# Optimization experiments

Measured on AMD Instinct MI355X. Metric: run time of the kernel, lower is better.

Reference implementation:

```python
import jax, jax.numpy as jnp
import numpy as np

L, B, N, DIM, H, DH, MLP = 2, 4, 2048, 768, 12, 64, 3072


def layer_norm(x, g, eps=1e-5):
    m = jnp.mean(x, axis=-1, keepdims=True)
    v = jnp.mean((x - m) ** 2, axis=-1, keepdims=True)
    return (x - m) / jnp.sqrt(v + eps) * g


def rms_norm(x, g):
    # F.normalize(x, dim=-1) * sqrt(dim_head) * gamma ; gamma: [H,1,DH]
    n = jnp.linalg.norm(x, axis=-1, keepdims=True)
    return x / jnp.maximum(n, 1e-12) * (x.shape[-1] ** 0.5) * g


def rotate_half(x):
    x1, x2 = jnp.split(x, 2, axis=-1)
    return jnp.concatenate([-x2, x1], axis=-1)


def apply_2d_rope(q, k, h_idx, w_idx):
    D = q.shape[-1]
    dq = D // 4
    inv_freq = 1.0 / (10000.0 ** (jnp.arange(dq, dtype=jnp.float32) / dq))

    def sincos(idx):
        th = idx[..., None].astype(jnp.float32) * inv_freq  # [B,N,dq]
        s = jnp.concatenate([jnp.sin(th), jnp.sin(th)], axis=-1)[:, None, :, :]
        c = jnp.concatenate([jnp.cos(th), jnp.cos(th)], axis=-1)[:, None, :, :]
        return s, c

    sh, ch = sincos(h_idx)
    sw, cw = sincos(w_idx)

    def rope(x, s, c):
        return x * c + rotate_half(x) * s

    dh = D // 2
    q = jnp.concatenate([rope(q[..., :dh], sh, ch), rope(q[..., dh:], sw, cw)], axis=-1)
    k = jnp.concatenate([rope(k[..., :dh], sh, ch), rope(k[..., dh:], sw, cw)], axis=-1)
    return q, k


def setup_inputs() -> dict:
    key = jax.random.key(0)
    ks = jax.random.split(key, 20)
    s = 0.02
    inp = {
        "patches": jax.random.normal(ks[0], (B, N, DIM), jnp.float32),
        "pe_ln1_g": jnp.ones((DIM,), jnp.float32),
        "pe_W": jax.random.normal(ks[1], (DIM, DIM), jnp.float32) * s,
        "pe_b": jnp.zeros((DIM,), jnp.float32),
        "pe_ln2_g": jnp.ones((DIM,), jnp.float32),
        "attn_ln_g": jnp.ones((L, DIM), jnp.float32),
        "qn_g": jnp.ones((L, H, 1, DH), jnp.float32),
        "kn_g": jnp.ones((L, H, 1, DH), jnp.float32),
        "Wq": jax.random.normal(ks[2], (L, DIM, H * DH), jnp.float32) * s,
        "Wkv": jax.random.normal(ks[3], (L, DIM, 2 * H * DH), jnp.float32) * s,
        "Wo": jax.random.normal(ks[4], (L, H * DH, DIM), jnp.float32) * s,
        "ff_ln_g": jnp.ones((L, DIM), jnp.float32),
        "W1": jax.random.normal(ks[5], (L, DIM, MLP), jnp.float32) * s,
        "b1": jnp.zeros((L, MLP), jnp.float32),
        "W2": jax.random.normal(ks[6], (L, MLP, DIM), jnp.float32) * s,
        "b2": jnp.zeros((L, DIM), jnp.float32),
        "final_ln_g": jnp.ones((DIM,), jnp.float32),
        "h_idx": jax.random.randint(ks[7], (B, N), 0, 64, jnp.int32),
        "w_idx": jax.random.randint(ks[8], (B, N), 0, 64, jnp.int32),
        "lengths": jax.random.randint(ks[9], (B,), 1, N + 1, jnp.int32),
    }
    return inp


def reference(patches, pe_ln1_g, pe_W, pe_b, pe_ln2_g, attn_ln_g, qn_g, kn_g,
              Wq, Wkv, Wo, ff_ln_g, W1, b1, W2, b2, final_ln_g,
              h_idx, w_idx, lengths):
    mask = jnp.arange(N)[None, :] < lengths[:, None]  # [B,N] validity mask
    # patch embedding: LN -> Linear -> LN
    x = layer_norm(patches, pe_ln1_g)
    x = x @ pe_W + pe_b
    x = layer_norm(x, pe_ln2_g)
    for i in range(L):
        xn = layer_norm(x, attn_ln_g[i])
        q = (xn @ Wq[i]).reshape(B, N, H, DH).transpose(0, 2, 1, 3)
        kv = xn @ Wkv[i]
        k = kv[..., : H * DH].reshape(B, N, H, DH).transpose(0, 2, 1, 3)
        v = kv[..., H * DH:].reshape(B, N, H, DH).transpose(0, 2, 1, 3)
        q = rms_norm(q, qn_g[i])
        k = rms_norm(k, kn_g[i])
        q, k = apply_2d_rope(q, k, h_idx, w_idx)
        dots = jnp.einsum('bhid,bhjd->bhij', q, k)  # no 1/sqrt(d): QK-RMSNorm supplies scale
        neg = -jnp.finfo(dots.dtype).max
        dots = jnp.where(mask[:, None, None, :], dots, neg)
        attn = jax.nn.softmax(dots, axis=-1)
        out = jnp.einsum('bhij,bhjd->bhid', attn, v)
        out = out.transpose(0, 2, 1, 3).reshape(B, N, H * DH)
        x = out @ Wo[i] + x
        h = layer_norm(x, ff_ln_g[i])
        h = jax.nn.gelu(h @ W1[i] + b1[i], approximate=False)
        x = h @ W2[i] + b2[i] + x
    x = layer_norm(x, final_ln_g)
    return x, mask
```

## Files before the change

kernel.cpp:

```cpp
#include <hip/hip_runtime.h>
#include <math.h>

#define LNUM 2
#define BB   4
#define NN   2048
#define DIM  768
#define NH   12
#define DH   64
#define MLPD 3072
#define QKVD 2304

typedef __attribute__((ext_vector_type(8))) short bf16x8;
typedef __attribute__((ext_vector_type(4))) float f32x4;
typedef unsigned short ushort_t;

__device__ __forceinline__ ushort_t f2bf(float f) {
    union { float f; unsigned u; } v; v.f = f;
    unsigned r = v.u + 0x7fff + ((v.u >> 16) & 1);
    return (ushort_t)(r >> 16);
}
__device__ __forceinline__ float bf2f(ushort_t s) {
    union { unsigned u; float f; } v; v.u = ((unsigned)s) << 16;
    return v.f;
}
__device__ __forceinline__ void gld16(const void* g, void* l) {
    __builtin_amdgcn_global_load_lds(
        (const __attribute__((address_space(1))) void*)g,
        (__attribute__((address_space(3))) void*)l, 16, 0, 0);
}
__device__ __forceinline__ float gelu_f(float x) {
    const float y = 0.7978845608028654f * (x + 0.044715f * x * x * x);
    const float t = 1.f - 2.f / (1.f + __expf(2.f * y));
    return 0.5f * x * (1.f + t);
}

#define WOFF_L 7077888
__global__ __launch_bounds__(256) void wconvert_all_kernel(
    const float* __restrict__ peW, const float* __restrict__ Wq,
    const float* __restrict__ Wkv, const float* __restrict__ Wo,
    const float* __restrict__ W1, const float* __restrict__ W2,
    ushort_t* __restrict__ wbf)
{
    int bid = blockIdx.x;
    const float* src; ushort_t* dst; int K, N;
    if (bid < 576)        { src = peW;                      dst = wbf;                               K = 768;  N = 768;  }
    else {
        bid -= 576;
        const int layer = bid / 6912;
        int t = bid % 6912;
        const size_t lw = (size_t)layer * WOFF_L;
        if (t < 576)        {           src = Wq  + (size_t)layer * 768 * 768;   dst = wbf + 589824 + lw;           K = 768;  N = 768;  }
        else if (t < 1728)  { t -= 576; src = Wkv + (size_t)layer * 768 * 1536;  dst = wbf + 589824 + 589824 + lw;  K = 768;  N = 1536; }
        else if (t < 2304)  { t -= 1728; src = Wo + (size_t)layer * 768 * 768;   dst = wbf + 589824 + 1769472 + lw; K = 768;  N = 768;  }
        else if (t < 4608)  { t -= 2304; src = W1 + (size_t)layer * 768 * 3072;  dst = wbf + 589824 + 2359296 + lw; K = 768;  N = 3072; }
        else                { t -= 4608; src = W2 + (size_t)layer * 3072 * 768;  dst = wbf + 589824 + 4718592 + lw; K = 3072; N = 768;  }
        bid = t;
    }
    const int tilesN = N / 32;
    const int nt = (bid % tilesN) * 32, kt = (bid / tilesN) * 32;

    __shared__ ushort_t tl[32][33];
    const int tx = threadIdx.x & 31, ty = threadIdx.x >> 5;
#pragma unroll
    for (int r = 0; r < 4; r++) {
        const int k = kt + ty + r * 8;
        tl[ty + r * 8][tx] = f2bf(src[(size_t)k * N + nt + tx]);
    }
    __syncthreads();
#pragma unroll
    for (int r = 0; r < 4; r++) {
        const int n = nt + ty + r * 8;
        dst[(size_t)n * K + kt + tx] = tl[tx][ty + r * 8];
    }
}

template <typename OT>
__global__ __launch_bounds__(256) void ln_kernel(const float* in, const float* g, OT* out)
{
    const int row = blockIdx.x;
    const int tid = threadIdx.x;
    const float* rp = in + (size_t)row * DIM;
    float vals[3];
    float s = 0.f, s2 = 0.f;
#pragma unroll
    for (int k = 0; k < 3; k++) {
        float v = rp[tid + k * 256];
        vals[k] = v;
        s += v; s2 += v * v;
    }
#pragma unroll
    for (int o = 32; o; o >>= 1) {
        s  += __shfl_xor(s, o);
        s2 += __shfl_xor(s2, o);
    }
    __shared__ float red[8];
    const int wid = tid >> 6;
    if ((tid & 63) == 0) { red[wid] = s; red[wid + 4] = s2; }
    __syncthreads();
    s  = red[0] + red[1] + red[2] + red[3];
    s2 = red[4] + red[5] + red[6] + red[7];
    const float mean = s * (1.f / DIM);
    const float var  = s2 * (1.f / DIM) - mean * mean;
    const float inv  = rsqrtf(var + 1e-5f);
    OT* op = out + (size_t)row * DIM;
#pragma unroll
    for (int k = 0; k < 3; k++) {
        const float v = (vals[k] - mean) * inv * g[tid + k * 256];
        if constexpr (sizeof(OT) == 2) op[tid + k * 256] = f2bf(v);
        else                           op[tid + k * 256] = v;
    }
}

template <int TM>
__global__ __launch_bounds__(256) void gemm_bf(
    const ushort_t* __restrict__ A, const ushort_t* __restrict__ Bt,
    const float* __restrict__ bias, const float* __restrict__ resid,
    void* __restrict__ Cv, int M, int N, int K, int outbf, int act)
{
    constexpr int MF = TM / 32;
    constexpr int AG = TM / 32;
    __shared__ ushort_t As[2][TM * 64];
    __shared__ ushort_t Bs[2][128 * 64];
    const int tid  = threadIdx.x;
    const int w    = tid >> 6, lane = tid & 63;
    const int lq   = lane & 15, quad = lane >> 4;
    const int wm   = w & 1, wn = w >> 1;
    const int tileM = blockIdx.y * TM, tileN = blockIdx.x * 128;

    const int srow   = lane >> 3;
    const int schunk = (lane & 7) ^ srow;
    const ushort_t* agp[AG];
    const ushort_t* bgp[4];
#pragma unroll
    for (int g = 0; g < AG; g++)
        agp[g] = A + (size_t)(tileM + g * 32 + w * 8 + srow) * K + schunk * 8;
#pragma unroll
    for (int g = 0; g < 4; g++)
        bgp[g] = Bt + (size_t)(tileN + g * 32 + w * 8 + srow) * K + schunk * 8;

    f32x4 acc[MF][4];
#pragma unroll
    for (int m = 0; m < MF; m++)
#pragma unroll
        for (int n = 0; n < 4; n++) acc[m][n] = (f32x4){0.f, 0.f, 0.f, 0.f};

    const int fsw0 = (quad ^ (lq & 7)) * 8;
    const int fsw1 = ((quad ^ (lq & 7)) ^ 4) * 8;

#pragma unroll
    for (int g = 0; g < AG; g++)
        gld16(agp[g], As[0] + (g * 32 + w * 8) * 64);
#pragma unroll
    for (int g = 0; g < 4; g++)
        gld16(bgp[g], Bs[0] + (g * 32 + w * 8) * 64);

    int buf = 0;
    for (int kt = 0; kt < K; kt += 64, buf ^= 1) {
        if (kt + 64 < K) {
#pragma unroll
            for (int g = 0; g < AG; g++)
                gld16(agp[g] + kt + 64, As[buf ^ 1] + (g * 32 + w * 8) * 64);
#pragma unroll
            for (int g = 0; g < 4; g++)
                gld16(bgp[g] + kt + 64, Bs[buf ^ 1] + (g * 32 + w * 8) * 64);
            if constexpr (TM == 128) asm volatile("s_waitcnt vmcnt(8)" ::: "memory");
            else                     asm volatile("s_waitcnt vmcnt(6)" ::: "memory");
        } else {
            asm volatile("s_waitcnt vmcnt(0)" ::: "memory");
        }
        __builtin_amdgcn_s_barrier();

        bf16x8 af0[MF], af1[MF], bf0[4], bf1[4];
#pragma unroll
        for (int m = 0; m < MF; m++) {
            const int base = ((wm * MF + m) * 16 + lq) * 64;
            af0[m] = *(const bf16x8*)&As[buf][base + fsw0];
            af1[m] = *(const bf16x8*)&As[buf][base + fsw1];
        }
#pragma unroll
        for (int n = 0; n < 4; n++) {
            const int base = ((wn * 4 + n) * 16 + lq) * 64;
            bf0[n] = *(const bf16x8*)&Bs[buf][base + fsw0];
            bf1[n] = *(const bf16x8*)&Bs[buf][base + fsw1];
        }
#pragma unroll
        for (int n = 0; n < 4; n++)
#pragma unroll
            for (int m = 0; m < MF; m++) {
                acc[m][n] = __builtin_amdgcn_mfma_f32_16x16x32_bf16(af0[m], bf0[n], acc[m][n], 0, 0, 0);
                acc[m][n] = __builtin_amdgcn_mfma_f32_16x16x32_bf16(af1[m], bf1[n], acc[m][n], 0, 0, 0);
            }
        __builtin_amdgcn_s_barrier();
    }

    float* Cf = (float*)Cv;
    ushort_t* Cb = (ushort_t*)Cv;
#pragma unroll
    for (int m = 0; m < MF; m++) {
#pragma unroll
        for (int n = 0; n < 4; n++) {
            const int col = tileN + wn * 64 + n * 16 + lq;
            const float bv = bias ? bias[col] : 0.f;
#pragma unroll
            for (int r = 0; r < 4; r++) {
                const int row = tileM + wm * (TM / 2) + m * 16 + quad * 4 + r;
                float v = acc[m][n][r] + bv;
                if (act) v = gelu_f(v);
                const size_t off = (size_t)row * N + col;
                if (resid) v += resid[off];
                if (outbf) Cb[off] = f2bf(v);
                else       Cf[off] = v;
            }
        }
    }
}

#define ASB(b) (Sh + (b) * 8192)
#define BSB(b) (Sh + 16384 + (b) * 8192)
__global__ __launch_bounds__(256) void gemm_qkv_kernel(
    const ushort_t* __restrict__ A, const ushort_t* __restrict__ Bt,
    ushort_t* __restrict__ C, ushort_t* __restrict__ Vt,
    const float* __restrict__ qg, const float* __restrict__ kg,
    const int* __restrict__ h_idx, const int* __restrict__ w_idx,
    int M, int N, int K)
{
    constexpr int MF = 4;
    constexpr int AG = 4;
    __shared__ ushort_t Sh[32768];
    const int tid  = threadIdx.x;
    const int w    = tid >> 6, lane = tid & 63;
    const int lq   = lane & 15, quad = lane >> 4;
    const int wm   = w & 1, wn = w >> 1;
    const int tileM = blockIdx.y * 128, tileN = blockIdx.x * 128;

    const int srow   = lane >> 3;
    const int schunk = (lane & 7) ^ srow;
    const ushort_t* agp[AG];
    const ushort_t* bgp[4];
#pragma unroll
    for (int g = 0; g < AG; g++)
        agp[g] = A + (size_t)(tileM + g * 32 + w * 8 + srow) * K + schunk * 8;
#pragma unroll
    for (int g = 0; g < 4; g++)
        bgp[g] = Bt + (size_t)(tileN + g * 32 + w * 8 + srow) * K + schunk * 8;

    f32x4 acc[MF][4];
#pragma unroll
    for (int m = 0; m < MF; m++)
#pragma unroll
        for (int n = 0; n < 4; n++) acc[m][n] = (f32x4){0.f, 0.f, 0.f, 0.f};

    const int fsw0 = (quad ^ (lq & 7)) * 8;
    const int fsw1 = ((quad ^ (lq & 7)) ^ 4) * 8;

#pragma unroll
    for (int g = 0; g < AG; g++)
        gld16(agp[g], ASB(0) + (g * 32 + w * 8) * 64);
#pragma unroll
    for (int g = 0; g < 4; g++)
        gld16(bgp[g], BSB(0) + (g * 32 + w * 8) * 64);

    int buf = 0;
    for (int kt = 0; kt < K; kt += 64, buf ^= 1) {
        if (kt + 64 < K) {
#pragma unroll
            for (int g = 0; g < AG; g++)
                gld16(agp[g] + kt + 64, ASB(buf ^ 1) + (g * 32 + w * 8) * 64);
#pragma unroll
            for (int g = 0; g < 4; g++)
                gld16(bgp[g] + kt + 64, BSB(buf ^ 1) + (g * 32 + w * 8) * 64);
            asm volatile("s_waitcnt vmcnt(8)" ::: "memory");
        } else {
            asm volatile("s_waitcnt vmcnt(0)" ::: "memory");
        }
        __builtin_amdgcn_s_barrier();

        bf16x8 af0[MF], af1[MF], bf0[4], bf1[4];
#pragma unroll
        for (int m = 0; m < MF; m++) {
            const int base = ((wm * MF + m) * 16 + lq) * 64;
            af0[m] = *(const bf16x8*)&ASB(buf)[base + fsw0];
            af1[m] = *(const bf16x8*)&ASB(buf)[base + fsw1];
        }
#pragma unroll
        for (int n = 0; n < 4; n++) {
            const int base = ((wn * 4 + n) * 16 + lq) * 64;
            bf0[n] = *(const bf16x8*)&BSB(buf)[base + fsw0];
            bf1[n] = *(const bf16x8*)&BSB(buf)[base + fsw1];
        }
#pragma unroll
        for (int n = 0; n < 4; n++)
#pragma unroll
            for (int m = 0; m < MF; m++) {
                acc[m][n] = __builtin_amdgcn_mfma_f32_16x16x32_bf16(af0[m], bf0[n], acc[m][n], 0, 0, 0);
                acc[m][n] = __builtin_amdgcn_mfma_f32_16x16x32_bf16(af1[m], bf1[n], acc[m][n], 0, 0, 0);
            }
        __builtin_amdgcn_s_barrier();
    }

    const int colb = tileN + wn * 64;
    if (colb >= 2 * DIM) {
        const int h0  = (tileN - 2 * DIM) >> 6;
        const int b   = tileM >> 11;
        const int nb0 = tileM & (NN - 1);
#pragma unroll
        for (int m = 0; m < MF; m++) {
            const int ns_loc = wm * 64 + m * 16 + quad * 4;
#pragma unroll
            for (int n = 0; n < 4; n++) {
                const int rowl = wn * 64 + n * 16 + lq;
                const unsigned lo = (unsigned)f2bf(acc[m][n][0]) | ((unsigned)f2bf(acc[m][n][1]) << 16);
                const unsigned hi = (unsigned)f2bf(acc[m][n][2]) | ((unsigned)f2bf(acc[m][n][3]) << 16);
                *(uint2*)&Sh[rowl * 136 + ns_loc] = make_uint2(lo, hi);
            }
        }
        __syncthreads();
        const int chunk = tid & 15;
        const int rgrp  = tid >> 4;
#pragma unroll
        for (int pr = 0; pr < 8; pr++) {
            const int rowl = pr * 16 + rgrp;
            const int hh = rowl >> 6, d = rowl & 63;
            const uint4 v4 = *(const uint4*)&Sh[rowl * 136 + chunk * 8];
            *(uint4*)&Vt[((size_t)(b * NH + h0 + hh) * DH + d) * NN + nb0 + chunk * 8] = v4;
        }
        return;
    }

    const float* gq = (colb < DIM) ? (qg + colb) : (kg + (colb - DIM));
    float gv4[4];
#pragma unroll
    for (int n = 0; n < 4; n++) gv4[n] = gq[n * 16 + lq];
    const float freq = exp2f((float)lq * -0.8304820237218407f);

#pragma unroll
    for (int m = 0; m < MF; m++) {
#pragma unroll
        for (int r = 0; r < 4; r++) {
            const int row = tileM + wm * 64 + m * 16 + quad * 4 + r;
            float v0 = acc[m][0][r], v1 = acc[m][1][r];
            float v2 = acc[m][2][r], v3 = acc[m][3][r];
            float ss = (v0 * v0 + v1 * v1) + (v2 * v2 + v3 * v3);
            ss += __shfl_xor(ss, 1);
            ss += __shfl_xor(ss, 2);
            ss += __shfl_xor(ss, 4);
            ss += __shfl_xor(ss, 8);
            const float sc = 8.0f / fmaxf(sqrtf(ss), 1e-12f);
            v0 *= sc * gv4[0]; v1 *= sc * gv4[1];
            v2 *= sc * gv4[2]; v3 *= sc * gv4[3];
            const float th1 = (float)h_idx[row] * freq;
            const float th2 = (float)w_idx[row] * freq;
            const float s1 = __sinf(th1), c1 = __cosf(th1);
            const float s2 = __sinf(th2), c2 = __cosf(th2);
            const float o0 = v0 * c1 - v1 * s1;
            const float o1 = v1 * c1 + v0 * s1;
            const float o2 = v2 * c2 - v3 * s2;
            const float o3 = v3 * c2 + v2 * s2;
            const size_t off = (size_t)row * N + colb + lq;
            C[off]      = f2bf(o0);
            C[off + 16] = f2bf(o1);
            C[off + 32] = f2bf(o2);
            C[off + 48] = f2bf(o3);
        }
    }
}

__global__ __launch_bounds__(256) void attn_kernel(
    const ushort_t* __restrict__ QKV, const ushort_t* __restrict__ Vt_g,
    const int* __restrict__ lengths, ushort_t* __restrict__ O)
{
    __shared__ ushort_t Ks[64 * 64];
    __shared__ ushort_t Vs[64 * 64];
    __shared__ ushort_t Ps[4][16][76];

    const int bh = blockIdx.x;
    const int b  = bh / NH;
    const int h  = bh % NH;
    const int qbase = blockIdx.y * 64;
    const int tid  = threadIdx.x;
    const int w    = tid >> 6;
    const int lane = tid & 63;
    const int lq   = lane & 15;
    const int quad = lane >> 4;
    const int len  = lengths[b];

    const int qrow = qbase + w * 16 + lq;
    const ushort_t* qp = QKV + (size_t)(b * NN + qrow) * QKVD + h * DH + quad * 8;
    bf16x8 aq0 = *(const bf16x8*)(qp);
    bf16x8 aq1 = *(const bf16x8*)(qp + 32);

    const int e0 = tid, e1 = tid + 256;
    const int r0 = e0 >> 3, c80 = e0 & 7;
    const int r1 = e1 >> 3, c81 = e1 & 7;
    const int g0 = (c80 ^ (r0 & 7) ^ (r0 >> 3)) & 7;
    const int g1 = (c81 ^ (r1 & 7) ^ (r1 >> 3)) & 7;
    const ushort_t* kg0 = QKV + (size_t)(b * NN + r0) * QKVD + DIM + h * DH + g0 * 8;
    const ushort_t* kg1 = QKV + (size_t)(b * NN + r1) * QKVD + DIM + h * DH + g1 * 8;
    const ushort_t* vg0 = Vt_g + ((size_t)(b * NH + h) * DH + r0) * NN + g0 * 8;
    const ushort_t* vg1 = Vt_g + ((size_t)(b * NH + h) * DH + r1) * NN + g1 * 8;
    ushort_t* kl0 = Ks + (w * 64) * 8;
    ushort_t* kl1 = Ks + (256 + w * 64) * 8;
    ushort_t* vl0 = Vs + (w * 64) * 8;
    ushort_t* vl1 = Vs + (256 + w * 64) * 8;

    f32x4 oacc[4];
#pragma unroll
    for (int t4 = 0; t4 < 4; t4++) oacc[t4] = (f32x4){0.f, 0.f, 0.f, 0.f};
    float lsum = 0.f;

    const int ntiles = (len + 63) >> 6;
    for (int t = 0; t < ntiles; t++) {
        const int j0 = t * 64;
        gld16(kg0 + (size_t)j0 * QKVD, kl0);
        gld16(kg1 + (size_t)j0 * QKVD, kl1);
        gld16(vg0 + j0, vl0);
        gld16(vg1 + j0, vl1);
        __syncthreads();

        f32x4 s[4];
#pragma unroll
        for (int n = 0; n < 4; n++) {
            const int krow = n * 16 + lq;
            const int hashk = (krow & 7) ^ (krow >> 3);
            bf16x8 ak0 = *(const bf16x8*)&Ks[(krow * 8 + ((quad ^ hashk) & 7)) * 8];
            bf16x8 ak1 = *(const bf16x8*)&Ks[(krow * 8 + (((quad + 4) ^ hashk) & 7)) * 8];
            f32x4 acc = (f32x4){0.f, 0.f, 0.f, 0.f};
            acc = __builtin_amdgcn_mfma_f32_16x16x32_bf16(ak0, aq0, acc, 0, 0, 0);
            acc = __builtin_amdgcn_mfma_f32_16x16x32_bf16(ak1, aq1, acc, 0, 0, 0);
            s[n] = acc;
        }

        float p[4][4];
#pragma unroll
        for (int n = 0; n < 4; n++) {
            const int keyb = j0 + n * 16 + quad * 4;
#pragma unroll
            for (int r = 0; r < 4; r++) {
                float pv = __expf(s[n][r]);
                pv = (keyb + r < len) ? pv : 0.f;
                p[n][r] = pv;
                lsum += pv;
            }
        }

#pragma unroll
        for (int n = 0; n < 4; n++) {
            const unsigned lo = (unsigned)f2bf(p[n][0]) | ((unsigned)f2bf(p[n][1]) << 16);
            const unsigned hi = (unsigned)f2bf(p[n][2]) | ((unsigned)f2bf(p[n][3]) << 16);
            *(uint2*)&Ps[w][lq][n * 16 + quad * 4] = make_uint2(lo, hi);
        }
        asm volatile("s_waitcnt lgkmcnt(0)" ::: "memory");
        bf16x8 ap0 = *(const bf16x8*)&Ps[w][lq][quad * 8];
        bf16x8 ap1 = *(const bf16x8*)&Ps[w][lq][32 + quad * 8];

#pragma unroll
        for (int t4 = 0; t4 < 4; t4++) {
            const int vrow = t4 * 16 + lq;
            const int hashv = (vrow & 7) ^ (vrow >> 3);
            bf16x8 bv0 = *(const bf16x8*)&Vs[(vrow * 8 + ((quad ^ hashv) & 7)) * 8];
            bf16x8 bv1 = *(const bf16x8*)&Vs[(vrow * 8 + (((quad + 4) ^ hashv) & 7)) * 8];
            oacc[t4] = __builtin_amdgcn_mfma_f32_16x16x32_bf16(ap0, bv0, oacc[t4], 0, 0, 0);
            oacc[t4] = __builtin_amdgcn_mfma_f32_16x16x32_bf16(ap1, bv1, oacc[t4], 0, 0, 0);
        }
        __syncthreads();
    }

    lsum += __shfl_xor(lsum, 16);
    lsum += __shfl_xor(lsum, 32);
    float invq[4];
#pragma unroll
    for (int r = 0; r < 4; r++) invq[r] = 1.f / __shfl(lsum, quad * 4 + r);

#pragma unroll
    for (int t4 = 0; t4 < 4; t4++) {
#pragma unroll
        for (int r = 0; r < 4; r++) {
            const int qr = qbase + w * 16 + quad * 4 + r;
            O[((size_t)(b * NN + qr)) * DIM + h * DH + t4 * 16 + lq] = f2bf(oacc[t4][r] * invq[r]);
        }
    }
}

__global__ __launch_bounds__(256) void mask_kernel(const int* __restrict__ lengths, float* __restrict__ out)
{
    const int i = blockIdx.x * 256 + threadIdx.x;
    const int b = i >> 11;
    const int n = i & (NN - 1);
    out[i] = (n < lengths[b]) ? 1.f : 0.f;
}

extern "C" void kernel_launch(void* const* d_in, const int* in_sizes, int n_in,
                              void* d_out, int out_size, void* d_ws, size_t ws_size,
                              hipStream_t stream)
{
    const float* patches    = (const float*)d_in[0];
    const float* pe_ln1_g   = (const float*)d_in[1];
    const float* pe_W       = (const float*)d_in[2];
    const float* pe_b       = (const float*)d_in[3];
    const float* pe_ln2_g   = (const float*)d_in[4];
    const float* attn_ln_g  = (const float*)d_in[5];
    const float* qn_g       = (const float*)d_in[6];
    const float* kn_g       = (const float*)d_in[7];
    const float* Wq         = (const float*)d_in[8];
    const float* Wkv        = (const float*)d_in[9];
    const float* Wo         = (const float*)d_in[10];
    const float* ff_ln_g    = (const float*)d_in[11];
    const float* W1         = (const float*)d_in[12];
    const float* b1         = (const float*)d_in[13];
    const float* W2         = (const float*)d_in[14];
    const float* b2         = (const float*)d_in[15];
    const float* final_ln_g = (const float*)d_in[16];
    const int*   h_idx      = (const int*)d_in[17];
    const int*   w_idx      = (const int*)d_in[18];
    const int*   lengths    = (const int*)d_in[19];

    float* out = (float*)d_out;
    char*  p   = (char*)d_ws;

    const size_t MB = 1024 * 1024;
    ushort_t* wbf = (ushort_t*)p;
    ushort_t* peWt = wbf;
    size_t woff = (size_t)DIM * DIM;
    ushort_t* Wqkvt[LNUM], *Wot[LNUM], *W1t[LNUM], *W2t[LNUM];
    for (int i = 0; i < LNUM; i++) {
        Wqkvt[i] = wbf + woff; woff += (size_t)QKVD * DIM;
        Wot[i]   = wbf + woff; woff += (size_t)DIM * DIM;
        W1t[i]   = wbf + woff; woff += (size_t)DIM * MLPD;
        W2t[i]   = wbf + woff; woff += (size_t)MLPD * DIM;
    }
    ushort_t* xnbf = (ushort_t*)(p + 30 * MB);
    ushort_t* qkv  = (ushort_t*)(p + 43 * MB);
    ushort_t* aob  = (ushort_t*)(p + 82 * MB);
    ushort_t* hb   = (ushort_t*)(p + 43 * MB);
    float*    peF  = (float*)(p + 43 * MB);
    ushort_t* vtg  = (ushort_t*)(p + 96 * MB);

    const int ROWS = BB * NN;
    dim3 blk(256);

    wconvert_all_kernel<<<dim3(576 + LNUM * 6912), blk, 0, stream>>>(
        pe_W, Wq, Wkv, Wo, W1, W2, wbf);

    ln_kernel<ushort_t><<<ROWS, blk, 0, stream>>>(patches, pe_ln1_g, xnbf);
    gemm_bf<64><<<dim3(DIM / 128, ROWS / 64), blk, 0, stream>>>(
        xnbf, peWt, pe_b, nullptr, peF, ROWS, DIM, DIM, 0, 0);
    ln_kernel<float><<<ROWS, blk, 0, stream>>>(peF, pe_ln2_g, out);

    float* x = out;
    for (int i = 0; i < LNUM; i++) {
        ln_kernel<ushort_t><<<ROWS, blk, 0, stream>>>(x, attn_ln_g + i * DIM, xnbf);
        gemm_qkv_kernel<<<dim3(QKVD / 128, ROWS / 128), blk, 0, stream>>>(
            xnbf, Wqkvt[i], qkv, vtg, qn_g + i * NH * DH, kn_g + i * NH * DH,
            h_idx, w_idx, ROWS, QKVD, DIM);
        attn_kernel<<<dim3(BB * NH, NN / 64), blk, 0, stream>>>(
            qkv, vtg, lengths, aob);
        gemm_bf<64><<<dim3(DIM / 128, ROWS / 64), blk, 0, stream>>>(
            aob, Wot[i], nullptr, x, x, ROWS, DIM, DIM, 0, 0);
        ln_kernel<ushort_t><<<ROWS, blk, 0, stream>>>(x, ff_ln_g + i * DIM, xnbf);
        gemm_bf<128><<<dim3(MLPD / 128, ROWS / 128), blk, 0, stream>>>(
            xnbf, W1t[i], b1 + i * MLPD, nullptr, hb, ROWS, MLPD, DIM, 1, 1);
        gemm_bf<64><<<dim3(DIM / 128, ROWS / 64), blk, 0, stream>>>(
            hb, W2t[i], b2 + i * DIM, x, x, ROWS, DIM, MLPD, 0, 0);
    }
    ln_kernel<float><<<ROWS, blk, 0, stream>>>(x, final_ln_g, out);
    mask_kernel<<<ROWS / 256, blk, 0, stream>>>(lengths, out + (size_t)ROWS * DIM);
}
```

Measured before the change: 840.1 us.

## Make attention kernel persistent with per-XCD atomic work queues

Replaces the 2D grid of attention blocks with 768 persistent blocks that pull work items from per-XCD atomic counters. Each XCD handles a fixed subset of (batch, head) pairs, so K/V reuse stays inside one XCD's L2, and dynamic claiming balances the variable-length work. This adds an atomic plus barrier per item and a memset launch before each attention call.

```diff
diff --git a/kernel.cpp b/kernel.cpp
--- a/kernel.cpp
+++ b/kernel.cpp
@@ -9,6 +9,9 @@
 #define DH   64
 #define MLPD 3072
 #define QKVD 2304
+
+#define ATTN_ITEMS_PER_XCD 192
+#define ATTN_BLOCKS        768
 
 typedef __attribute__((ext_vector_type(8))) short bf16x8;
 typedef __attribute__((ext_vector_type(4))) float f32x4;
@@ -367,117 +370,131 @@
 
 __global__ __launch_bounds__(256) void attn_kernel(
     const ushort_t* __restrict__ QKV, const ushort_t* __restrict__ Vt_g,
-    const int* __restrict__ lengths, ushort_t* __restrict__ O)
+    const int* __restrict__ lengths, ushort_t* __restrict__ O,
+    unsigned* __restrict__ ctrs)
 {
     __shared__ ushort_t Ks[64 * 64];
     __shared__ ushort_t Vs[64 * 64];
     __shared__ ushort_t Ps[4][16][76];
-
-    const int bh = blockIdx.x;
-    const int b  = bh / NH;
-    const int h  = bh % NH;
-    const int qbase = blockIdx.y * 64;
+    __shared__ int s_item;
+
     const int tid  = threadIdx.x;
     const int w    = tid >> 6;
     const int lane = tid & 63;
     const int lq   = lane & 15;
     const int quad = lane >> 4;
-    const int len  = lengths[b];
-
-    const int qrow = qbase + w * 16 + lq;
-    const ushort_t* qp = QKV + (size_t)(b * NN + qrow) * QKVD + h * DH + quad * 8;
-    bf16x8 aq0 = *(const bf16x8*)(qp);
-    bf16x8 aq1 = *(const bf16x8*)(qp + 32);
+    const int xcd  = blockIdx.x & 7;
 
     const int e0 = tid, e1 = tid + 256;
     const int r0 = e0 >> 3, c80 = e0 & 7;
     const int r1 = e1 >> 3, c81 = e1 & 7;
     const int g0 = (c80 ^ (r0 & 7) ^ (r0 >> 3)) & 7;
     const int g1 = (c81 ^ (r1 & 7) ^ (r1 >> 3)) & 7;
-    const ushort_t* kg0 = QKV + (size_t)(b * NN + r0) * QKVD + DIM + h * DH + g0 * 8;
-    const ushort_t* kg1 = QKV + (size_t)(b * NN + r1) * QKVD + DIM + h * DH + g1 * 8;
-    const ushort_t* vg0 = Vt_g + ((size_t)(b * NH + h) * DH + r0) * NN + g0 * 8;
-    const ushort_t* vg1 = Vt_g + ((size_t)(b * NH + h) * DH + r1) * NN + g1 * 8;
     ushort_t* kl0 = Ks + (w * 64) * 8;
     ushort_t* kl1 = Ks + (256 + w * 64) * 8;
     ushort_t* vl0 = Vs + (w * 64) * 8;
     ushort_t* vl1 = Vs + (256 + w * 64) * 8;
 
-    f32x4 oacc[4];
-#pragma unroll
-    for (int t4 = 0; t4 < 4; t4++) oacc[t4] = (f32x4){0.f, 0.f, 0.f, 0.f};
-    float lsum = 0.f;
-
-    const int ntiles = (len + 63) >> 6;
-    for (int t = 0; t < ntiles; t++) {
-        const int j0 = t * 64;
-        gld16(kg0 + (size_t)j0 * QKVD, kl0);
-        gld16(kg1 + (size_t)j0 * QKVD, kl1);
-        gld16(vg0 + j0, vl0);
-        gld16(vg1 + j0, vl1);
+    for (;;) {
+        if (tid == 0) s_item = (int)atomicAdd(&ctrs[xcd], 1u);
         __syncthreads();
-
-        f32x4 s[4];
-#pragma unroll
-        for (int n = 0; n < 4; n++) {
-            const int krow = n * 16 + lq;
-            const int hashk = (krow & 7) ^ (krow >> 3);
-            bf16x8 ak0 = *(const bf16x8*)&Ks[(krow * 8 + ((quad ^ hashk) & 7)) * 8];
-            bf16x8 ak1 = *(const bf16x8*)&Ks[(krow * 8 + (((quad + 4) ^ hashk) & 7)) * 8];
-            f32x4 acc = (f32x4){0.f, 0.f, 0.f, 0.f};
-            acc = __builtin_amdgcn_mfma_f32_16x16x32_bf16(ak0, aq0, acc, 0, 0, 0);
-            acc = __builtin_amdgcn_mfma_f32_16x16x32_bf16(ak1, aq1, acc, 0, 0, 0);
-            s[n] = acc;
-        }
-
-        float p[4][4];
-#pragma unroll
-        for (int n = 0; n < 4; n++) {
-            const int keyb = j0 + n * 16 + quad * 4;
+        const int j = s_item;
+        if (j >= ATTN_ITEMS_PER_XCD) break;
+
+        const int bh    = xcd + 8 * (j % 6);
+        const int qbase = (j / 6) * 64;
+        const int b     = bh / NH;
+        const int h     = bh % NH;
+        const int len   = lengths[b];
+
+        const int qrow = qbase + w * 16 + lq;
+        const ushort_t* qp = QKV + (size_t)(b * NN + qrow) * QKVD + h * DH + quad * 8;
+        bf16x8 aq0 = *(const bf16x8*)(qp);
+        bf16x8 aq1 = *(const bf16x8*)(qp + 32);
+
+        const ushort_t* kg0 = QKV + (size_t)(b * NN + r0) * QKVD + DIM + h * DH + g0 * 8;
+        const ushort_t* kg1 = QKV + (size_t)(b * NN + r1) * QKVD + DIM + h * DH + g1 * 8;
+        const ushort_t* vg0 = Vt_g + ((size_t)(b * NH + h) * DH + r0) * NN + g0 * 8;
+        const ushort_t* vg1 = Vt_g + ((size_t)(b * NH + h) * DH + r1) * NN + g1 * 8;
+
+        f32x4 oacc[4];
+#pragma unroll
+        for (int t4 = 0; t4 < 4; t4++) oacc[t4] = (f32x4){0.f, 0.f, 0.f, 0.f};
+        float lsum = 0.f;
+
+        const int ntiles = (len + 63) >> 6;
+        for (int t = 0; t < ntiles; t++) {
+            const int j0 = t * 64;
+            gld16(kg0 + (size_t)j0 * QKVD, kl0);
+            gld16(kg1 + (size_t)j0 * QKVD, kl1);
+            gld16(vg0 + j0, vl0);
+            gld16(vg1 + j0, vl1);
+            __syncthreads();
+
+            f32x4 s[4];
+#pragma unroll
+            for (int n = 0; n < 4; n++) {
+                const int krow = n * 16 + lq;
+                const int hashk = (krow & 7) ^ (krow >> 3);
+                bf16x8 ak0 = *(const bf16x8*)&Ks[(krow * 8 + ((quad ^ hashk) & 7)) * 8];
+                bf16x8 ak1 = *(const bf16x8*)&Ks[(krow * 8 + (((quad + 4) ^ hashk) & 7)) * 8];
+                f32x4 acc = (f32x4){0.f, 0.f, 0.f, 0.f};
+                acc = __builtin_amdgcn_mfma_f32_16x16x32_bf16(ak0, aq0, acc, 0, 0, 0);
+                acc = __builtin_amdgcn_mfma_f32_16x16x32_bf16(ak1, aq1, acc, 0, 0, 0);
+                s[n] = acc;
+            }
+
+            float p[4][4];
+#pragma unroll
+            for (int n = 0; n < 4; n++) {
+                const int keyb = j0 + n * 16 + quad * 4;
+#pragma unroll
+                for (int r = 0; r < 4; r++) {
+                    float pv = __expf(s[n][r]);
+                    pv = (keyb + r < len) ? pv : 0.f;
+                    p[n][r] = pv;
+                    lsum += pv;
+                }
+            }
+
+#pragma unroll
+            for (int n = 0; n < 4; n++) {
+                const unsigned lo = (unsigned)f2bf(p[n][0]) | ((unsigned)f2bf(p[n][1]) << 16);
+                const unsigned hi = (unsigned)f2bf(p[n][2]) | ((unsigned)f2bf(p[n][3]) << 16);
+                *(uint2*)&Ps[w][lq][n * 16 + quad * 4] = make_uint2(lo, hi);
+            }
+            asm volatile("s_waitcnt lgkmcnt(0)" ::: "memory");
+            bf16x8 ap0 = *(const bf16x8*)&Ps[w][lq][quad * 8];
+            bf16x8 ap1 = *(const bf16x8*)&Ps[w][lq][32 + quad * 8];
+
+#pragma unroll
+            for (int t4 = 0; t4 < 4; t4++) {
+                const int vrow = t4 * 16 + lq;
+                const int hashv = (vrow & 7) ^ (vrow >> 3);
+                bf16x8 bv0 = *(const bf16x8*)&Vs[(vrow * 8 + ((quad ^ hashv) & 7)) * 8];
+                bf16x8 bv1 = *(const bf16x8*)&Vs[(vrow * 8 + (((quad + 4) ^ hashv) & 7)) * 8];
+                oacc[t4] = __builtin_amdgcn_mfma_f32_16x16x32_bf16(ap0, bv0, oacc[t4], 0, 0, 0);
+                oacc[t4] = __builtin_amdgcn_mfma_f32_16x16x32_bf16(ap1, bv1, oacc[t4], 0, 0, 0);
+            }
+            __syncthreads();
+        }
+
+        float ls = lsum;
+        ls += __shfl_xor(ls, 16);
+        ls += __shfl_xor(ls, 32);
+        float invq[4];
+#pragma unroll
+        for (int r = 0; r < 4; r++) invq[r] = 1.f / __shfl(ls, quad * 4 + r);
+
+#pragma unroll
+        for (int t4 = 0; t4 < 4; t4++) {
 #pragma unroll
             for (int r = 0; r < 4; r++) {
-                float pv = __expf(s[n][r]);
-                pv = (keyb + r < len) ? pv : 0.f;
-                p[n][r] = pv;
-                lsum += pv;
-            }
-        }
-
-#pragma unroll
-        for (int n = 0; n < 4; n++) {
-            const unsigned lo = (unsigned)f2bf(p[n][0]) | ((unsigned)f2bf(p[n][1]) << 16);
-            const unsigned hi = (unsigned)f2bf(p[n][2]) | ((unsigned)f2bf(p[n][3]) << 16);
-            *(uint2*)&Ps[w][lq][n * 16 + quad * 4] = make_uint2(lo, hi);
-        }
-        asm volatile("s_waitcnt lgkmcnt(0)" ::: "memory");
-        bf16x8 ap0 = *(const bf16x8*)&Ps[w][lq][quad * 8];
-        bf16x8 ap1 = *(const bf16x8*)&Ps[w][lq][32 + quad * 8];
-
-#pragma unroll
-        for (int t4 = 0; t4 < 4; t4++) {
-            const int vrow = t4 * 16 + lq;
-            const int hashv = (vrow & 7) ^ (vrow >> 3);
-            bf16x8 bv0 = *(const bf16x8*)&Vs[(vrow * 8 + ((quad ^ hashv) & 7)) * 8];
-            bf16x8 bv1 = *(const bf16x8*)&Vs[(vrow * 8 + (((quad + 4) ^ hashv) & 7)) * 8];
-            oacc[t4] = __builtin_amdgcn_mfma_f32_16x16x32_bf16(ap0, bv0, oacc[t4], 0, 0, 0);
-            oacc[t4] = __builtin_amdgcn_mfma_f32_16x16x32_bf16(ap1, bv1, oacc[t4], 0, 0, 0);
+                const int qr = qbase + w * 16 + quad * 4 + r;
+                O[((size_t)(b * NN + qr)) * DIM + h * DH + t4 * 16 + lq] = f2bf(oacc[t4][r] * invq[r]);
+            }
         }
         __syncthreads();
-    }
-
-    lsum += __shfl_xor(lsum, 16);
-    lsum += __shfl_xor(lsum, 32);
-    float invq[4];
-#pragma unroll
-    for (int r = 0; r < 4; r++) invq[r] = 1.f / __shfl(lsum, quad * 4 + r);
-
-#pragma unroll
-    for (int t4 = 0; t4 < 4; t4++) {
-#pragma unroll
-        for (int r = 0; r < 4; r++) {
-            const int qr = qbase + w * 16 + quad * 4 + r;
-            O[((size_t)(b * NN + qr)) * DIM + h * DH + t4 * 16 + lq] = f2bf(oacc[t4][r] * invq[r]);
-        }
     }
 }
 
@@ -528,6 +545,7 @@
         W1t[i]   = wbf + woff; woff += (size_t)DIM * MLPD;
         W2t[i]   = wbf + woff; woff += (size_t)MLPD * DIM;
     }
+    unsigned* ctrs = (unsigned*)(p + 29 * MB);
     ushort_t* xnbf = (ushort_t*)(p + 30 * MB);
     ushort_t* qkv  = (ushort_t*)(p + 43 * MB);
     ushort_t* aob  = (ushort_t*)(p + 82 * MB);
@@ -552,8 +570,9 @@
         gemm_qkv_kernel<<<dim3(QKVD / 128, ROWS / 128), blk, 0, stream>>>(
             xnbf, Wqkvt[i], qkv, vtg, qn_g + i * NH * DH, kn_g + i * NH * DH,
             h_idx, w_idx, ROWS, QKVD, DIM);
-        attn_kernel<<<dim3(BB * NH, NN / 64), blk, 0, stream>>>(
-            qkv, vtg, lengths, aob);
+        hipMemsetAsync(ctrs, 0, 8 * sizeof(unsigned), stream);
+        attn_kernel<<<dim3(ATTN_BLOCKS), blk, 0, stream>>>(
+            qkv, vtg, lengths, aob, ctrs);
         gemm_bf<64><<<dim3(DIM / 128, ROWS / 64), blk, 0, stream>>>(
             aob, Wot[i], nullptr, x, x, ROWS, DIM, DIM, 0, 0);
         ln_kernel<ushort_t><<<ROWS, blk, 0, stream>>>(x, ff_ln_g + i * DIM, xnbf);
```

Measured after the change: 863.9 us. 2.8% more time.
